# Performance work log

Measured on AMD Instinct MI355X. Metric: run time of the kernel, lower is better.

The kernel has to match this reference:

```python
import jax, jax.numpy as jnp
import numpy as np

N_NODES = 100000
N_EDGES = 1600000
IN_DIM = 128
HIDDEN = 128
OUT_DIM = 64


def setup_inputs() -> dict:
    key = jax.random.key(0)
    k_x, k_e, k_w1, k_b1, k_w2, k_b2 = jax.random.split(key, 6)
    x = jax.random.normal(k_x, (N_NODES, IN_DIM), dtype=jnp.float32)
    edge_index = jax.random.randint(k_e, (2, N_EDGES), 0, N_NODES, dtype=jnp.int64)
    # GCNConv weight/bias (glorot-ish scale) and final Linear head
    W1 = jax.random.normal(k_w1, (IN_DIM, HIDDEN), dtype=jnp.float32) / np.sqrt(IN_DIM)
    b1 = jnp.zeros((HIDDEN,), dtype=jnp.float32)
    W2 = jax.random.normal(k_w2, (HIDDEN, OUT_DIM), dtype=jnp.float32) / np.sqrt(HIDDEN)
    b2 = jnp.zeros((OUT_DIM,), dtype=jnp.float32)
    return {"x": x, "W1": W1, "b1": b1, "W2": W2, "b2": b2, "edge_index": edge_index}


def _gcn_conv(x, W, b, src, dst, norm, n_nodes):
    # PyG GCNConv: linear transform, then sym-normalized neighbor aggregation
    h = x @ W                                   # (N, H) dense transform
    msg = h[src] * norm[:, None]                # (E+N, H) gather + scale
    out = jax.ops.segment_sum(msg, dst, num_segments=n_nodes)  # scatter-add
    return out + b


def reference(x, W1, b1, W2, b2, edge_index):
    n = x.shape[0]
    # add self-loops (PyG GCNConv default)
    loop = jnp.arange(n, dtype=edge_index.dtype)
    src = jnp.concatenate([edge_index[0], loop])
    dst = jnp.concatenate([edge_index[1], loop])
    # symmetric normalization D^{-1/2} A D^{-1/2}
    deg = jnp.zeros((n,), dtype=x.dtype).at[dst].add(1.0)
    dinv = jnp.where(deg > 0, jax.lax.rsqrt(jnp.maximum(deg, 1.0)), 0.0)
    norm = dinv[src] * dinv[dst]

    h = _gcn_conv(x, W1, b1, src, dst, norm, n)
    h = jax.nn.relu(h)
    # dropout: identity in eval/inference mode
    return h @ W2 + b2
```

## Files before the change

### kernel.cpp

```cpp
#include <hip/hip_runtime.h>

#define N_NODES 100000
#define N_EDGES 1600000
#define IN_DIM  128
#define HIDDEN  128
#define OUT_DIM 64

#define NB_COARSE ((N_NODES + 255) / 256)
#define EPB 4096
#define NBLK_E ((N_EDGES + EPB - 1) / EPB)
#define CAP 5120
#define PCAP 6912

typedef __attribute__((ext_vector_type(8))) short bf8_t;
typedef __attribute__((ext_vector_type(4))) float f4_t;

__device__ __forceinline__ ushort f2b(float f) {
    unsigned int u = __float_as_uint(f);
    u += 0x7fffu + ((u >> 16) & 1u);
    return (ushort)(u >> 16);
}
__device__ __forceinline__ float b2f_lo(unsigned int u) { return __uint_as_float(u << 16); }
__device__ __forceinline__ float b2f_hi(unsigned int u) { return __uint_as_float(u & 0xffff0000u); }


__global__ void k_zero(int* __restrict__ cursor, unsigned int* __restrict__ hz) {
    int t = threadIdx.x;
    if (t < NB_COARSE) cursor[t] = t * CAP;
    if (t >= NB_COARSE && t < NB_COARSE + 64)
        hz[(size_t)N_NODES * 64 + (t - NB_COARSE)] = 0u;
}


__global__ __launch_bounds__(256) void k_part(const int* __restrict__ ei,
                                              int* __restrict__ cursor,
                                              unsigned int* __restrict__ part) {
    __shared__ int lh[NB_COARSE];
    __shared__ int lbase[NB_COARSE];
    int t = threadIdx.x;
    for (int i = t; i < NB_COARSE; i += 256) lh[i] = 0;
    __syncthreads();
    int e0 = blockIdx.x * EPB;
    int srcv[EPB / 256], dstv[EPB / 256];
    #pragma unroll
    for (int j = 0; j < EPB / 256; j++) {
        int e = e0 + j * 256 + t;
        if (e < N_EDGES) {
            srcv[j] = ei[e];
            dstv[j] = ei[N_EDGES + e];
            atomicAdd(&lh[dstv[j] >> 8], 1);
        } else dstv[j] = -1;
    }
    __syncthreads();
    for (int i = t; i < NB_COARSE; i += 256) {
        int c = lh[i];
        lbase[i] = (c > 0) ? atomicAdd(&cursor[i], c) : 0;
        lh[i] = 0;
    }
    __syncthreads();
    #pragma unroll
    for (int j = 0; j < EPB / 256; j++) {
        if (dstv[j] >= 0) {
            int b = dstv[j] >> 8;
            int pos = lbase[b] + atomicAdd(&lh[b], 1);
            part[pos] = ((unsigned int)(dstv[j] & 255) << 24) | (unsigned int)srcv[j];
        }
    }
}


__global__ __launch_bounds__(256) void k_csr(const unsigned int* __restrict__ part,
                                             const int* __restrict__ cursor,
                                             int* __restrict__ offs,
                                             int* __restrict__ pcnt,
                                             float* __restrict__ dinv,
                                             int* __restrict__ ssrc) {
    __shared__ int ldeg[256], lsc[256], lcur[256], sob[256];
    __shared__ unsigned int stage[CAP];
    int t = threadIdx.x;
    int b = blockIdx.x;
    int rbeg = b * CAP;
    int cnt = cursor[b] - rbeg;
    int node0 = b << 8;
    ldeg[t] = 0;
    __syncthreads();
    for (int i = t; i < cnt; i += 256) {
        unsigned int u = part[rbeg + i];
        stage[i] = u;
        atomicAdd(&ldeg[u >> 24], 1);
    }
    __syncthreads();
    int v = ldeg[t];
    int pv = (v + 7) & ~7;
    lsc[t] = pv;
    __syncthreads();
    for (int off = 1; off < 256; off <<= 1) {
        int add = (t >= off) ? lsc[t - off] : 0;
        __syncthreads();
        lsc[t] += add;
        __syncthreads();
    }
    int ob = b * PCAP + (lsc[t] - pv);
    sob[t] = ob;
    lcur[t] = 0;
    if (node0 + t < N_NODES) {
        offs[node0 + t] = ob;
        pcnt[node0 + t] = pv;
        dinv[node0 + t] = rsqrtf((float)(v + 1));
    }
    __syncthreads();
    for (int i = t; i < cnt; i += 256) {
        unsigned int u = stage[i];
        int d = u >> 24;
        int pos = atomicAdd(&lcur[d], 1);
        ssrc[sob[d] + pos] = (int)(u & 0xFFFFFFu);
    }
    for (int i = v; i < pv; i++) ssrc[ob + i] = N_NODES;
}


template <int BN, bool A_BF16, bool OUT_BF16>
__global__ __launch_bounds__(256, 2) void k_mfma(const void* __restrict__ Av,
                                                 const float* __restrict__ W,
                                                 const float* __restrict__ bias,
                                                 const float* __restrict__ dinv,
                                                 void* __restrict__ Cv, int M) {
    constexpr int BM = 128, KK = 128, PAD = 8;
    constexpr int MF = (BN == 128) ? 4 : 2;
    constexpr int NF = 4;
    __shared__ ushort As[BM][KK + PAD];
    __shared__ ushort Bs[BN][KK + PAD];

    int tid = threadIdx.x;
    int row0 = blockIdx.x * BM;

    if (A_BF16) {
        const ushort* A = (const ushort*)Av;
        #pragma unroll
        for (int i = 0; i < 8; i++) {
            int li = tid + i * 256;
            int r = li >> 4, c8 = li & 15;
            int grow = row0 + r; if (grow > M - 1) grow = M - 1;
            uint4 v = *(const uint4*)(A + (size_t)grow * KK + c8 * 8);
            *(uint4*)&As[r][c8 * 8] = v;
        }
    } else {
        const float* A = (const float*)Av;
        #pragma unroll
        for (int i = 0; i < 16; i++) {
            int li = tid + i * 256;
            int r = li >> 5, c4 = li & 31;
            int grow = row0 + r; if (grow > M - 1) grow = M - 1;
            float4 v = *(const float4*)(A + (size_t)grow * KK + c4 * 4);
            ushort4 o;
            o.x = f2b(v.x); o.y = f2b(v.y); o.z = f2b(v.z); o.w = f2b(v.w);
            *(ushort4*)&As[r][c4 * 4] = o;
        }
    }
    #pragma unroll
    for (int i = 0; i < (KK * BN / 4) / 256; i++) {
        int li = tid + i * 256;
        int k = li / (BN / 4), n4 = li % (BN / 4);
        float4 v = *(const float4*)(W + (size_t)k * BN + n4 * 4);
        Bs[n4 * 4 + 0][k] = f2b(v.x);
        Bs[n4 * 4 + 1][k] = f2b(v.y);
        Bs[n4 * 4 + 2][k] = f2b(v.z);
        Bs[n4 * 4 + 3][k] = f2b(v.w);
    }
    __syncthreads();

    int wave = tid >> 6, lane = tid & 63;
    int lr = lane & 15, lq = lane >> 4;
    int wm0 = (BN == 128) ? (wave & 1) * 64 : wave * 32;
    int wn0 = (BN == 128) ? (wave >> 1) * 64 : 0;

    f4_t acc[MF][NF];
    #pragma unroll
    for (int mi = 0; mi < MF; mi++)
        #pragma unroll
        for (int ni = 0; ni < NF; ni++) acc[mi][ni] = (f4_t){0.f, 0.f, 0.f, 0.f};

    #pragma unroll
    for (int kb = 0; kb < 4; kb++) {
        bf8_t af[MF], bfr[NF];
        #pragma unroll
        for (int mi = 0; mi < MF; mi++)
            af[mi] = *(const bf8_t*)&As[wm0 + mi * 16 + lr][kb * 32 + lq * 8];
        #pragma unroll
        for (int ni = 0; ni < NF; ni++)
            bfr[ni] = *(const bf8_t*)&Bs[wn0 + ni * 16 + lr][kb * 32 + lq * 8];
        #pragma unroll
        for (int mi = 0; mi < MF; mi++)
            #pragma unroll
            for (int ni = 0; ni < NF; ni++)
                acc[mi][ni] = __builtin_amdgcn_mfma_f32_16x16x32_bf16(
                    af[mi], bfr[ni], acc[mi][ni], 0, 0, 0);
    }

    #pragma unroll
    for (int mi = 0; mi < MF; mi++) {
        #pragma unroll
        for (int r = 0; r < 4; r++) {
            int row = row0 + wm0 + mi * 16 + lq * 4 + r;
            if (row < M) {
                if (OUT_BF16) {
                    float dv = dinv[row];
                    ushort* C = (ushort*)Cv;
                    #pragma unroll
                    for (int ni = 0; ni < NF; ni++)
                        C[(size_t)row * BN + wn0 + ni * 16 + lr] = f2b(acc[mi][ni][r] * dv);
                } else {
                    float* C = (float*)Cv;
                    #pragma unroll
                    for (int ni = 0; ni < NF; ni++) {
                        int col = wn0 + ni * 16 + lr;
                        C[(size_t)row * BN + col] = acc[mi][ni][r] + bias[col];
                    }
                }
            }
        }
    }
}


__global__ __launch_bounds__(256) void k_agg(const ushort* __restrict__ h,
                                             const int* __restrict__ offs,
                                             const int* __restrict__ pcnt,
                                             const int* __restrict__ ssrc,
                                             const float* __restrict__ dinv,
                                             const float* __restrict__ b1,
                                             ushort* __restrict__ h2) {
    int wave = threadIdx.x >> 6;
    int lane = threadIdx.x & 63;
    int n = blockIdx.x * 4 + wave;
    if (n >= N_NODES) return;

    const unsigned int* hp = (const unsigned int*)h;
    int e0 = offs[n];
    int iters = pcnt[n] >> 3;
    const uint4* ip = (const uint4*)(ssrc + e0);

    float ax0 = 0.f, ay0 = 0.f, ax1 = 0.f, ay1 = 0.f;
    float ax2 = 0.f, ay2 = 0.f, ax3 = 0.f, ay3 = 0.f;
    uint4 i0, i1;
    if (iters > 0) { i0 = ip[0]; i1 = ip[1]; }
    for (int it = 0; it < iters; it++) {
        uint4 nx0 = i0, nx1 = i1;
        if (it + 1 < iters) { nx0 = ip[(it + 1) * 2]; nx1 = ip[(it + 1) * 2 + 1]; }
        unsigned int u0 = hp[i0.x * 64 + lane];
        unsigned int u1 = hp[i0.y * 64 + lane];
        unsigned int u2 = hp[i0.z * 64 + lane];
        unsigned int u3 = hp[i0.w * 64 + lane];
        unsigned int u4 = hp[i1.x * 64 + lane];
        unsigned int u5 = hp[i1.y * 64 + lane];
        unsigned int u6 = hp[i1.z * 64 + lane];
        unsigned int u7 = hp[i1.w * 64 + lane];
        ax0 += b2f_lo(u0); ay0 += b2f_hi(u0);
        ax1 += b2f_lo(u1); ay1 += b2f_hi(u1);
        ax2 += b2f_lo(u2); ay2 += b2f_hi(u2);
        ax3 += b2f_lo(u3); ay3 += b2f_hi(u3);
        ax0 += b2f_lo(u4); ay0 += b2f_hi(u4);
        ax1 += b2f_lo(u5); ay1 += b2f_hi(u5);
        ax2 += b2f_lo(u6); ay2 += b2f_hi(u6);
        ax3 += b2f_lo(u7); ay3 += b2f_hi(u7);
        i0 = nx0; i1 = nx1;
    }
    unsigned int us = hp[(size_t)n * 64 + lane];
    float dn = dinv[n];
    float rx = (ax0 + ax1 + ax2 + ax3 + b2f_lo(us)) * dn;
    float ry = (ay0 + ay1 + ay2 + ay3 + b2f_hi(us)) * dn;
    float2 bb = ((const float2*)b1)[lane];
    rx += bb.x; ry += bb.y;
    rx = rx > 0.f ? rx : 0.f;
    ry = ry > 0.f ? ry : 0.f;
    unsigned int o = ((unsigned int)f2b(ry) << 16) | (unsigned int)f2b(rx);
    ((unsigned int*)h2)[(size_t)n * 64 + lane] = o;
}


extern "C" void kernel_launch(void* const* d_in, const int* in_sizes, int n_in,
                              void* d_out, int out_size, void* d_ws, size_t ws_size,
                              hipStream_t stream) {
    const float* x  = (const float*)d_in[0];
    const float* W1 = (const float*)d_in[1];
    const float* b1 = (const float*)d_in[2];
    const float* W2 = (const float*)d_in[3];
    const float* b2 = (const float*)d_in[4];
    const int*   ei = (const int*)d_in[5];
    float* out = (float*)d_out;

    char* w = (char*)d_ws;
    size_t off = 0;
    auto alloc = [&](size_t bytes) -> void* {
        void* p = w + off;
        off += (bytes + 255) & ~(size_t)255;
        return p;
    };
    ushort* h      = (ushort*)alloc((size_t)(N_NODES + 1) * HIDDEN * 2);
    ushort* h2     = (ushort*)alloc((size_t)N_NODES * HIDDEN * 2);
    float* dinv    = (float*)alloc((size_t)N_NODES * 4);
    int*   offs    = (int*)alloc((size_t)N_NODES * 4);
    int*   pcnt    = (int*)alloc((size_t)N_NODES * 4);
    int*   ssrc    = (int*)alloc((size_t)NB_COARSE * PCAP * 4);
    unsigned int* part = (unsigned int*)alloc((size_t)NB_COARSE * CAP * 4);
    int*   cursor  = (int*)alloc((size_t)NB_COARSE * 4);

    k_zero<<<1, 512, 0, stream>>>(cursor, (unsigned int*)h);
    k_part<<<NBLK_E, 256, 0, stream>>>(ei, cursor, part);
    k_csr<<<NB_COARSE, 256, 0, stream>>>(part, cursor, offs, pcnt, dinv, ssrc);

    k_mfma<HIDDEN, false, true><<<(N_NODES + 127) / 128, 256, 0, stream>>>(
        x, W1, nullptr, dinv, h, N_NODES);
    k_agg<<<(N_NODES + 3) / 4, 256, 0, stream>>>(h, offs, pcnt, ssrc, dinv, b1, h2);
    k_mfma<OUT_DIM, true, false><<<(N_NODES + 127) / 128, 256, 0, stream>>>(
        h2, W2, b2, nullptr, out, N_NODES);
}
```

Before: 235.8 us.

## Fuse neighbor aggregation with the output linear layer via shared memory

The aggregation kernel and the second GEMM are merged into one kernel. Each 512-thread block aggregates 128 nodes, 16 per wave, and writes the bf16 ReLU results into shared memory. It then runs MFMA against W2 in place and writes the final output. This removes the h2 intermediate round trip through global memory and one kernel launch. In exchange, the grid shrinks to about 782 blocks that each process nodes serially, which lowers the number of gathers in flight and can unbalance load across blocks.

```diff
diff --git a/kernel.cpp b/kernel.cpp
--- a/kernel.cpp
+++ b/kernel.cpp
@@ -119,48 +119,31 @@
 }
 
 
-template <int BN, bool A_BF16, bool OUT_BF16>
-__global__ __launch_bounds__(256, 2) void k_mfma(const void* __restrict__ Av,
-                                                 const float* __restrict__ W,
-                                                 const float* __restrict__ bias,
-                                                 const float* __restrict__ dinv,
-                                                 void* __restrict__ Cv, int M) {
-    constexpr int BM = 128, KK = 128, PAD = 8;
-    constexpr int MF = (BN == 128) ? 4 : 2;
-    constexpr int NF = 4;
+__global__ __launch_bounds__(256, 2) void k_mfma1(const float* __restrict__ A,
+                                                  const float* __restrict__ W,
+                                                  const float* __restrict__ dinv,
+                                                  ushort* __restrict__ C, int M) {
+    constexpr int BM = 128, KK = 128, PAD = 8, BN = 128, MF = 4, NF = 4;
     __shared__ ushort As[BM][KK + PAD];
     __shared__ ushort Bs[BN][KK + PAD];
 
     int tid = threadIdx.x;
     int row0 = blockIdx.x * BM;
 
-    if (A_BF16) {
-        const ushort* A = (const ushort*)Av;
-        #pragma unroll
-        for (int i = 0; i < 8; i++) {
-            int li = tid + i * 256;
-            int r = li >> 4, c8 = li & 15;
-            int grow = row0 + r; if (grow > M - 1) grow = M - 1;
-            uint4 v = *(const uint4*)(A + (size_t)grow * KK + c8 * 8);
-            *(uint4*)&As[r][c8 * 8] = v;
-        }
-    } else {
-        const float* A = (const float*)Av;
-        #pragma unroll
-        for (int i = 0; i < 16; i++) {
-            int li = tid + i * 256;
-            int r = li >> 5, c4 = li & 31;
-            int grow = row0 + r; if (grow > M - 1) grow = M - 1;
-            float4 v = *(const float4*)(A + (size_t)grow * KK + c4 * 4);
-            ushort4 o;
-            o.x = f2b(v.x); o.y = f2b(v.y); o.z = f2b(v.z); o.w = f2b(v.w);
-            *(ushort4*)&As[r][c4 * 4] = o;
-        }
-    }
-    #pragma unroll
-    for (int i = 0; i < (KK * BN / 4) / 256; i++) {
+    #pragma unroll
+    for (int i = 0; i < 16; i++) {
         int li = tid + i * 256;
-        int k = li / (BN / 4), n4 = li % (BN / 4);
+        int r = li >> 5, c4 = li & 31;
+        int grow = row0 + r; if (grow > M - 1) grow = M - 1;
+        float4 v = *(const float4*)(A + (size_t)grow * KK + c4 * 4);
+        ushort4 o;
+        o.x = f2b(v.x); o.y = f2b(v.y); o.z = f2b(v.z); o.w = f2b(v.w);
+        *(ushort4*)&As[r][c4 * 4] = o;
+    }
+    #pragma unroll
+    for (int i = 0; i < 16; i++) {
+        int li = tid + i * 256;
+        int k = li >> 5, n4 = li & 31;
         float4 v = *(const float4*)(W + (size_t)k * BN + n4 * 4);
         Bs[n4 * 4 + 0][k] = f2b(v.x);
         Bs[n4 * 4 + 1][k] = f2b(v.y);
@@ -171,8 +154,8 @@
 
     int wave = tid >> 6, lane = tid & 63;
     int lr = lane & 15, lq = lane >> 4;
-    int wm0 = (BN == 128) ? (wave & 1) * 64 : wave * 32;
-    int wn0 = (BN == 128) ? (wave >> 1) * 64 : 0;
+    int wm0 = (wave & 1) * 64;
+    int wn0 = (wave >> 1) * 64;
 
     f4_t acc[MF][NF];
     #pragma unroll
@@ -203,78 +186,114 @@
         for (int r = 0; r < 4; r++) {
             int row = row0 + wm0 + mi * 16 + lq * 4 + r;
             if (row < M) {
-                if (OUT_BF16) {
-                    float dv = dinv[row];
-                    ushort* C = (ushort*)Cv;
-                    #pragma unroll
-                    for (int ni = 0; ni < NF; ni++)
-                        C[(size_t)row * BN + wn0 + ni * 16 + lr] = f2b(acc[mi][ni][r] * dv);
-                } else {
-                    float* C = (float*)Cv;
-                    #pragma unroll
-                    for (int ni = 0; ni < NF; ni++) {
-                        int col = wn0 + ni * 16 + lr;
-                        C[(size_t)row * BN + col] = acc[mi][ni][r] + bias[col];
-                    }
-                }
+                float dv = dinv[row];
+                #pragma unroll
+                for (int ni = 0; ni < NF; ni++)
+                    C[(size_t)row * BN + wn0 + ni * 16 + lr] = f2b(acc[mi][ni][r] * dv);
             }
         }
     }
 }
 
 
-__global__ __launch_bounds__(256) void k_agg(const ushort* __restrict__ h,
-                                             const int* __restrict__ offs,
-                                             const int* __restrict__ pcnt,
-                                             const int* __restrict__ ssrc,
-                                             const float* __restrict__ dinv,
-                                             const float* __restrict__ b1,
-                                             ushort* __restrict__ h2) {
-    int wave = threadIdx.x >> 6;
-    int lane = threadIdx.x & 63;
-    int n = blockIdx.x * 4 + wave;
-    if (n >= N_NODES) return;
+__global__ __launch_bounds__(512, 6) void k_aggmm(const ushort* __restrict__ h,
+                                                  const int* __restrict__ offs,
+                                                  const int* __restrict__ pcnt,
+                                                  const int* __restrict__ ssrc,
+                                                  const float* __restrict__ dinv,
+                                                  const float* __restrict__ b1,
+                                                  const float* __restrict__ W2,
+                                                  const float* __restrict__ b2,
+                                                  float* __restrict__ out, int M) {
+    constexpr int BM = 128, KK = 128, PAD = 8, BN = 64;
+    __shared__ ushort As[BM][KK + PAD];
+    __shared__ ushort Bs[BN][KK + PAD];
+
+    int tid = threadIdx.x;
+    int wave = tid >> 6, lane = tid & 63;
+    int row0 = blockIdx.x * BM;
+
+    #pragma unroll
+    for (int i = 0; i < 4; i++) {
+        int li = tid + i * 512;
+        int k = li >> 4, n4 = li & 15;
+        float4 v = *(const float4*)(W2 + (size_t)k * BN + n4 * 4);
+        Bs[n4 * 4 + 0][k] = f2b(v.x);
+        Bs[n4 * 4 + 1][k] = f2b(v.y);
+        Bs[n4 * 4 + 2][k] = f2b(v.z);
+        Bs[n4 * 4 + 3][k] = f2b(v.w);
+    }
 
     const unsigned int* hp = (const unsigned int*)h;
-    int e0 = offs[n];
-    int iters = pcnt[n] >> 3;
-    const uint4* ip = (const uint4*)(ssrc + e0);
-
-    float ax0 = 0.f, ay0 = 0.f, ax1 = 0.f, ay1 = 0.f;
-    float ax2 = 0.f, ay2 = 0.f, ax3 = 0.f, ay3 = 0.f;
-    uint4 i0, i1;
-    if (iters > 0) { i0 = ip[0]; i1 = ip[1]; }
-    for (int it = 0; it < iters; it++) {
-        uint4 nx0 = i0, nx1 = i1;
-        if (it + 1 < iters) { nx0 = ip[(it + 1) * 2]; nx1 = ip[(it + 1) * 2 + 1]; }
-        unsigned int u0 = hp[i0.x * 64 + lane];
-        unsigned int u1 = hp[i0.y * 64 + lane];
-        unsigned int u2 = hp[i0.z * 64 + lane];
-        unsigned int u3 = hp[i0.w * 64 + lane];
-        unsigned int u4 = hp[i1.x * 64 + lane];
-        unsigned int u5 = hp[i1.y * 64 + lane];
-        unsigned int u6 = hp[i1.z * 64 + lane];
-        unsigned int u7 = hp[i1.w * 64 + lane];
-        ax0 += b2f_lo(u0); ay0 += b2f_hi(u0);
-        ax1 += b2f_lo(u1); ay1 += b2f_hi(u1);
-        ax2 += b2f_lo(u2); ay2 += b2f_hi(u2);
-        ax3 += b2f_lo(u3); ay3 += b2f_hi(u3);
-        ax0 += b2f_lo(u4); ay0 += b2f_hi(u4);
-        ax1 += b2f_lo(u5); ay1 += b2f_hi(u5);
-        ax2 += b2f_lo(u6); ay2 += b2f_hi(u6);
-        ax3 += b2f_lo(u7); ay3 += b2f_hi(u7);
-        i0 = nx0; i1 = nx1;
-    }
-    unsigned int us = hp[(size_t)n * 64 + lane];
-    float dn = dinv[n];
-    float rx = (ax0 + ax1 + ax2 + ax3 + b2f_lo(us)) * dn;
-    float ry = (ay0 + ay1 + ay2 + ay3 + b2f_hi(us)) * dn;
     float2 bb = ((const float2*)b1)[lane];
-    rx += bb.x; ry += bb.y;
-    rx = rx > 0.f ? rx : 0.f;
-    ry = ry > 0.f ? ry : 0.f;
-    unsigned int o = ((unsigned int)f2b(ry) << 16) | (unsigned int)f2b(rx);
-    ((unsigned int*)h2)[(size_t)n * 64 + lane] = o;
+    #pragma unroll 1
+    for (int nn = 0; nn < 16; nn++) {
+        int r = wave * 16 + nn;
+        int n = row0 + r;
+        if (n >= M) break;
+        int e0 = offs[n];
+        int iters = pcnt[n] >> 3;
+        const uint4* ip = (const uint4*)(ssrc + e0);
+
+        float2 a0 = {0.f, 0.f}, a1 = {0.f, 0.f}, a2 = {0.f, 0.f}, a3 = {0.f, 0.f};
+        uint4 i0, i1;
+        if (iters > 0) { i0 = ip[0]; i1 = ip[1]; }
+        for (int it = 0; it < iters; it++) {
+            uint4 nx0 = i0, nx1 = i1;
+            if (it + 1 < iters) { nx0 = ip[(it + 1) * 2]; nx1 = ip[(it + 1) * 2 + 1]; }
+            unsigned int u0 = hp[i0.x * 64 + lane];
+            unsigned int u1 = hp[i0.y * 64 + lane];
+            unsigned int u2 = hp[i0.z * 64 + lane];
+            unsigned int u3 = hp[i0.w * 64 + lane];
+            unsigned int u4 = hp[i1.x * 64 + lane];
+            unsigned int u5 = hp[i1.y * 64 + lane];
+            unsigned int u6 = hp[i1.z * 64 + lane];
+            unsigned int u7 = hp[i1.w * 64 + lane];
+            a0.x += b2f_lo(u0); a0.y += b2f_hi(u0);
+            a1.x += b2f_lo(u1); a1.y += b2f_hi(u1);
+            a2.x += b2f_lo(u2); a2.y += b2f_hi(u2);
+            a3.x += b2f_lo(u3); a3.y += b2f_hi(u3);
+            a0.x += b2f_lo(u4); a0.y += b2f_hi(u4);
+            a1.x += b2f_lo(u5); a1.y += b2f_hi(u5);
+            a2.x += b2f_lo(u6); a2.y += b2f_hi(u6);
+            a3.x += b2f_lo(u7); a3.y += b2f_hi(u7);
+            i0 = nx0; i1 = nx1;
+        }
+        unsigned int us = hp[(size_t)n * 64 + lane];
+        float dn = dinv[n];
+        float rx = (a0.x + a1.x + a2.x + a3.x + b2f_lo(us)) * dn + bb.x;
+        float ry = (a0.y + a1.y + a2.y + a3.y + b2f_hi(us)) * dn + bb.y;
+        rx = rx > 0.f ? rx : 0.f;
+        ry = ry > 0.f ? ry : 0.f;
+        unsigned int o = ((unsigned int)f2b(ry) << 16) | (unsigned int)f2b(rx);
+        *(unsigned int*)&As[r][lane * 2] = o;
+    }
+    __syncthreads();
+
+    int lr = lane & 15, lq = lane >> 4;
+    f4_t acc[4];
+    #pragma unroll
+    for (int ni = 0; ni < 4; ni++) acc[ni] = (f4_t){0.f, 0.f, 0.f, 0.f};
+    #pragma unroll
+    for (int kb = 0; kb < 4; kb++) {
+        bf8_t af = *(const bf8_t*)&As[wave * 16 + lr][kb * 32 + lq * 8];
+        #pragma unroll
+        for (int ni = 0; ni < 4; ni++) {
+            bf8_t bf = *(const bf8_t*)&Bs[ni * 16 + lr][kb * 32 + lq * 8];
+            acc[ni] = __builtin_amdgcn_mfma_f32_16x16x32_bf16(af, bf, acc[ni], 0, 0, 0);
+        }
+    }
+    #pragma unroll
+    for (int r = 0; r < 4; r++) {
+        int row = row0 + wave * 16 + lq * 4 + r;
+        if (row < M) {
+            #pragma unroll
+            for (int ni = 0; ni < 4; ni++) {
+                int col = ni * 16 + lr;
+                out[(size_t)row * BN + col] = acc[ni][r] + b2[col];
+            }
+        }
+    }
 }
 
 
@@ -297,7 +316,6 @@
         return p;
     };
     ushort* h      = (ushort*)alloc((size_t)(N_NODES + 1) * HIDDEN * 2);
-    ushort* h2     = (ushort*)alloc((size_t)N_NODES * HIDDEN * 2);
     float* dinv    = (float*)alloc((size_t)N_NODES * 4);
     int*   offs    = (int*)alloc((size_t)N_NODES * 4);
     int*   pcnt    = (int*)alloc((size_t)N_NODES * 4);
@@ -309,9 +327,7 @@
     k_part<<<NBLK_E, 256, 0, stream>>>(ei, cursor, part);
     k_csr<<<NB_COARSE, 256, 0, stream>>>(part, cursor, offs, pcnt, dinv, ssrc);
 
-    k_mfma<HIDDEN, false, true><<<(N_NODES + 127) / 128, 256, 0, stream>>>(
-        x, W1, nullptr, dinv, h, N_NODES);
-    k_agg<<<(N_NODES + 3) / 4, 256, 0, stream>>>(h, offs, pcnt, ssrc, dinv, b1, h2);
-    k_mfma<OUT_DIM, true, false><<<(N_NODES + 127) / 128, 256, 0, stream>>>(
-        h2, W2, b2, nullptr, out, N_NODES);
-}
+    k_mfma1<<<(N_NODES + 127) / 128, 256, 0, stream>>>(x, W1, dinv, h, N_NODES);
+    k_aggmm<<<(N_NODES + 127) / 128, 512, 0, stream>>>(h, offs, pcnt, ssrc, dinv,
+                                                       b1, W2, b2, out, N_NODES);
+}
```

New measurement: 255.6 us. +8.4%, slower.

## Fuse edge partitioning with first GEMM and move source-side normalization into aggregation

Applied to the files above, without the earlier changes.

The edge-partition kernel and the first X@W1 GEMM are merged into one launch that assigns blocks to either task, so the GEMM no longer waits for the CSR build and the two run concurrently. To allow that, the GEMM no longer scales rows by dinv. The aggregation kernel now gathers dinv[src] per neighbor and applies it with an FMA, and the self-loop term gets dinv applied twice. The zero-init kernel becomes a memset, and padding now relies on dinv[N_NODES]=0 instead of a zeroed h row. The cost is an extra random dinv gather per edge in the aggregation hot loop.

```diff
diff --git a/kernel.cpp b/kernel.cpp
--- a/kernel.cpp
+++ b/kernel.cpp
@@ -9,6 +9,7 @@
 #define NB_COARSE ((N_NODES + 255) / 256)
 #define EPB 4096
 #define NBLK_E ((N_EDGES + EPB - 1) / EPB)
+#define GB1 ((N_NODES + 127) / 128)
 #define CAP 5120
 #define PCAP 6912
 
@@ -24,46 +25,115 @@
 __device__ __forceinline__ float b2f_hi(unsigned int u) { return __uint_as_float(u & 0xffff0000u); }
 
 
-__global__ void k_zero(int* __restrict__ cursor, unsigned int* __restrict__ hz) {
-    int t = threadIdx.x;
-    if (t < NB_COARSE) cursor[t] = t * CAP;
-    if (t >= NB_COARSE && t < NB_COARSE + 64)
-        hz[(size_t)N_NODES * 64 + (t - NB_COARSE)] = 0u;
-}
-
-
-__global__ __launch_bounds__(256) void k_part(const int* __restrict__ ei,
-                                              int* __restrict__ cursor,
-                                              unsigned int* __restrict__ part) {
-    __shared__ int lh[NB_COARSE];
-    __shared__ int lbase[NB_COARSE];
-    int t = threadIdx.x;
-    for (int i = t; i < NB_COARSE; i += 256) lh[i] = 0;
-    __syncthreads();
-    int e0 = blockIdx.x * EPB;
-    int srcv[EPB / 256], dstv[EPB / 256];
-    #pragma unroll
-    for (int j = 0; j < EPB / 256; j++) {
-        int e = e0 + j * 256 + t;
-        if (e < N_EDGES) {
-            srcv[j] = ei[e];
-            dstv[j] = ei[N_EDGES + e];
-            atomicAdd(&lh[dstv[j] >> 8], 1);
-        } else dstv[j] = -1;
-    }
-    __syncthreads();
-    for (int i = t; i < NB_COARSE; i += 256) {
-        int c = lh[i];
-        lbase[i] = (c > 0) ? atomicAdd(&cursor[i], c) : 0;
-        lh[i] = 0;
-    }
-    __syncthreads();
-    #pragma unroll
-    for (int j = 0; j < EPB / 256; j++) {
-        if (dstv[j] >= 0) {
-            int b = dstv[j] >> 8;
-            int pos = lbase[b] + atomicAdd(&lh[b], 1);
-            part[pos] = ((unsigned int)(dstv[j] & 255) << 24) | (unsigned int)srcv[j];
+__global__ __launch_bounds__(256, 2) void k_fuse1(const int* __restrict__ ei,
+                                                  int* __restrict__ cursor,
+                                                  unsigned int* __restrict__ part,
+                                                  const float* __restrict__ x,
+                                                  const float* __restrict__ W1,
+                                                  ushort* __restrict__ h) {
+    __shared__ __align__(16) ushort smem[2 * 128 * 136];
+    int tid = threadIdx.x;
+
+    if (blockIdx.x < NBLK_E) {
+        int* lh    = (int*)smem;
+        int* lbase = lh + NB_COARSE;
+        for (int i = tid; i < NB_COARSE; i += 256) lh[i] = 0;
+        __syncthreads();
+        int e0 = blockIdx.x * EPB;
+        int srcv[EPB / 256], dstv[EPB / 256];
+        #pragma unroll
+        for (int j = 0; j < EPB / 256; j++) {
+            int e = e0 + j * 256 + tid;
+            if (e < N_EDGES) {
+                srcv[j] = ei[e];
+                dstv[j] = ei[N_EDGES + e];
+                atomicAdd(&lh[dstv[j] >> 8], 1);
+            } else dstv[j] = -1;
+        }
+        __syncthreads();
+        for (int i = tid; i < NB_COARSE; i += 256) {
+            int c = lh[i];
+            lbase[i] = (c > 0) ? (i * CAP + atomicAdd(&cursor[i], c)) : 0;
+            lh[i] = 0;
+        }
+        __syncthreads();
+        #pragma unroll
+        for (int j = 0; j < EPB / 256; j++) {
+            if (dstv[j] >= 0) {
+                int b = dstv[j] >> 8;
+                int pos = lbase[b] + atomicAdd(&lh[b], 1);
+                part[pos] = ((unsigned int)(dstv[j] & 255) << 24) | (unsigned int)srcv[j];
+            }
+        }
+        return;
+    }
+
+    typedef ushort (*tile_t)[136];
+    tile_t As = (tile_t)smem;
+    tile_t Bs = (tile_t)(smem + 128 * 136);
+    int row0 = (blockIdx.x - NBLK_E) * 128;
+    const int M = N_NODES;
+
+    #pragma unroll
+    for (int i = 0; i < 16; i++) {
+        int li = tid + i * 256;
+        int r = li >> 5, c4 = li & 31;
+        int grow = row0 + r; if (grow > M - 1) grow = M - 1;
+        float4 v = *(const float4*)(x + (size_t)grow * 128 + c4 * 4);
+        ushort4 o;
+        o.x = f2b(v.x); o.y = f2b(v.y); o.z = f2b(v.z); o.w = f2b(v.w);
+        *(ushort4*)&As[r][c4 * 4] = o;
+    }
+    #pragma unroll
+    for (int i = 0; i < 16; i++) {
+        int li = tid + i * 256;
+        int k = li >> 5, n4 = li & 31;
+        float4 v = *(const float4*)(W1 + (size_t)k * 128 + n4 * 4);
+        Bs[n4 * 4 + 0][k] = f2b(v.x);
+        Bs[n4 * 4 + 1][k] = f2b(v.y);
+        Bs[n4 * 4 + 2][k] = f2b(v.z);
+        Bs[n4 * 4 + 3][k] = f2b(v.w);
+    }
+    __syncthreads();
+
+    int wave = tid >> 6, lane = tid & 63;
+    int lr = lane & 15, lq = lane >> 4;
+    int wm0 = (wave & 1) * 64;
+    int wn0 = (wave >> 1) * 64;
+
+    f4_t acc[4][4];
+    #pragma unroll
+    for (int mi = 0; mi < 4; mi++)
+        #pragma unroll
+        for (int ni = 0; ni < 4; ni++) acc[mi][ni] = (f4_t){0.f, 0.f, 0.f, 0.f};
+
+    #pragma unroll
+    for (int kb = 0; kb < 4; kb++) {
+        bf8_t af[4], bfr[4];
+        #pragma unroll
+        for (int mi = 0; mi < 4; mi++)
+            af[mi] = *(const bf8_t*)&As[wm0 + mi * 16 + lr][kb * 32 + lq * 8];
+        #pragma unroll
+        for (int ni = 0; ni < 4; ni++)
+            bfr[ni] = *(const bf8_t*)&Bs[wn0 + ni * 16 + lr][kb * 32 + lq * 8];
+        #pragma unroll
+        for (int mi = 0; mi < 4; mi++)
+            #pragma unroll
+            for (int ni = 0; ni < 4; ni++)
+                acc[mi][ni] = __builtin_amdgcn_mfma_f32_16x16x32_bf16(
+                    af[mi], bfr[ni], acc[mi][ni], 0, 0, 0);
+    }
+
+    #pragma unroll
+    for (int mi = 0; mi < 4; mi++) {
+        #pragma unroll
+        for (int r = 0; r < 4; r++) {
+            int row = row0 + wm0 + mi * 16 + lq * 4 + r;
+            if (row < M) {
+                #pragma unroll
+                for (int ni = 0; ni < 4; ni++)
+                    h[(size_t)row * 128 + wn0 + ni * 16 + lr] = f2b(acc[mi][ni][r]);
+            }
         }
     }
 }
@@ -80,8 +150,9 @@
     int t = threadIdx.x;
     int b = blockIdx.x;
     int rbeg = b * CAP;
-    int cnt = cursor[b] - rbeg;
+    int cnt = cursor[b];
     int node0 = b << 8;
+    if (b == 0 && t == 0) dinv[N_NODES] = 0.f;
     ldeg[t] = 0;
     __syncthreads();
     for (int i = t; i < cnt; i += 256) {
@@ -116,110 +187,6 @@
         ssrc[sob[d] + pos] = (int)(u & 0xFFFFFFu);
     }
     for (int i = v; i < pv; i++) ssrc[ob + i] = N_NODES;
-}
-
-
-template <int BN, bool A_BF16, bool OUT_BF16>
-__global__ __launch_bounds__(256, 2) void k_mfma(const void* __restrict__ Av,
-                                                 const float* __restrict__ W,
-                                                 const float* __restrict__ bias,
-                                                 const float* __restrict__ dinv,
-                                                 void* __restrict__ Cv, int M) {
-    constexpr int BM = 128, KK = 128, PAD = 8;
-    constexpr int MF = (BN == 128) ? 4 : 2;
-    constexpr int NF = 4;
-    __shared__ ushort As[BM][KK + PAD];
-    __shared__ ushort Bs[BN][KK + PAD];
-
-    int tid = threadIdx.x;
-    int row0 = blockIdx.x * BM;
-
-    if (A_BF16) {
-        const ushort* A = (const ushort*)Av;
-        #pragma unroll
-        for (int i = 0; i < 8; i++) {
-            int li = tid + i * 256;
-            int r = li >> 4, c8 = li & 15;
-            int grow = row0 + r; if (grow > M - 1) grow = M - 1;
-            uint4 v = *(const uint4*)(A + (size_t)grow * KK + c8 * 8);
-            *(uint4*)&As[r][c8 * 8] = v;
-        }
-    } else {
-        const float* A = (const float*)Av;
-        #pragma unroll
-        for (int i = 0; i < 16; i++) {
-            int li = tid + i * 256;
-            int r = li >> 5, c4 = li & 31;
-            int grow = row0 + r; if (grow > M - 1) grow = M - 1;
-            float4 v = *(const float4*)(A + (size_t)grow * KK + c4 * 4);
-            ushort4 o;
-            o.x = f2b(v.x); o.y = f2b(v.y); o.z = f2b(v.z); o.w = f2b(v.w);
-            *(ushort4*)&As[r][c4 * 4] = o;
-        }
-    }
-    #pragma unroll
-    for (int i = 0; i < (KK * BN / 4) / 256; i++) {
-        int li = tid + i * 256;
-        int k = li / (BN / 4), n4 = li % (BN / 4);
-        float4 v = *(const float4*)(W + (size_t)k * BN + n4 * 4);
-        Bs[n4 * 4 + 0][k] = f2b(v.x);
-        Bs[n4 * 4 + 1][k] = f2b(v.y);
-        Bs[n4 * 4 + 2][k] = f2b(v.z);
-        Bs[n4 * 4 + 3][k] = f2b(v.w);
-    }
-    __syncthreads();
-
-    int wave = tid >> 6, lane = tid & 63;
-    int lr = lane & 15, lq = lane >> 4;
-    int wm0 = (BN == 128) ? (wave & 1) * 64 : wave * 32;
-    int wn0 = (BN == 128) ? (wave >> 1) * 64 : 0;
-
-    f4_t acc[MF][NF];
-    #pragma unroll
-    for (int mi = 0; mi < MF; mi++)
-        #pragma unroll
-        for (int ni = 0; ni < NF; ni++) acc[mi][ni] = (f4_t){0.f, 0.f, 0.f, 0.f};
-
-    #pragma unroll
-    for (int kb = 0; kb < 4; kb++) {
-        bf8_t af[MF], bfr[NF];
-        #pragma unroll
-        for (int mi = 0; mi < MF; mi++)
-            af[mi] = *(const bf8_t*)&As[wm0 + mi * 16 + lr][kb * 32 + lq * 8];
-        #pragma unroll
-        for (int ni = 0; ni < NF; ni++)
-            bfr[ni] = *(const bf8_t*)&Bs[wn0 + ni * 16 + lr][kb * 32 + lq * 8];
-        #pragma unroll
-        for (int mi = 0; mi < MF; mi++)
-            #pragma unroll
-            for (int ni = 0; ni < NF; ni++)
-                acc[mi][ni] = __builtin_amdgcn_mfma_f32_16x16x32_bf16(
-                    af[mi], bfr[ni], acc[mi][ni], 0, 0, 0);
-    }
-
-    #pragma unroll
-    for (int mi = 0; mi < MF; mi++) {
-        #pragma unroll
-        for (int r = 0; r < 4; r++) {
-            int row = row0 + wm0 + mi * 16 + lq * 4 + r;
-            if (row < M) {
-                if (OUT_BF16) {
-                    float dv = dinv[row];
-                    ushort* C = (ushort*)Cv;
-                    #pragma unroll
-                    for (int ni = 0; ni < NF; ni++)
-                        C[(size_t)row * BN + wn0 + ni * 16 + lr] = f2b(acc[mi][ni][r] * dv);
-                } else {
-                    float* C = (float*)Cv;
-                    #pragma unroll
-                    for (int ni = 0; ni < NF; ni++) {
-                        int col = wn0 + ni * 16 + lr;
-                        C[(size_t)row * BN + col] = acc[mi][ni][r] + bias[col];
-                    }
-                }
-            }
-        }
-    }
 }
 
 
@@ -247,6 +214,8 @@
     for (int it = 0; it < iters; it++) {
         uint4 nx0 = i0, nx1 = i1;
         if (it + 1 < iters) { nx0 = ip[(it + 1) * 2]; nx1 = ip[(it + 1) * 2 + 1]; }
+        float w0 = dinv[i0.x], w1 = dinv[i0.y], w2 = dinv[i0.z], w3 = dinv[i0.w];
+        float w4 = dinv[i1.x], w5 = dinv[i1.y], w6 = dinv[i1.z], w7 = dinv[i1.w];
         unsigned int u0 = hp[i0.x * 64 + lane];
         unsigned int u1 = hp[i0.y * 64 + lane];
         unsigned int u2 = hp[i0.z * 64 + lane];
@@ -255,26 +224,101 @@
         unsigned int u5 = hp[i1.y * 64 + lane];
         unsigned int u6 = hp[i1.z * 64 + lane];
         unsigned int u7 = hp[i1.w * 64 + lane];
-        ax0 += b2f_lo(u0); ay0 += b2f_hi(u0);
-        ax1 += b2f_lo(u1); ay1 += b2f_hi(u1);
-        ax2 += b2f_lo(u2); ay2 += b2f_hi(u2);
-        ax3 += b2f_lo(u3); ay3 += b2f_hi(u3);
-        ax0 += b2f_lo(u4); ay0 += b2f_hi(u4);
-        ax1 += b2f_lo(u5); ay1 += b2f_hi(u5);
-        ax2 += b2f_lo(u6); ay2 += b2f_hi(u6);
-        ax3 += b2f_lo(u7); ay3 += b2f_hi(u7);
+        ax0 = fmaf(b2f_lo(u0), w0, ax0); ay0 = fmaf(b2f_hi(u0), w0, ay0);
+        ax1 = fmaf(b2f_lo(u1), w1, ax1); ay1 = fmaf(b2f_hi(u1), w1, ay1);
+        ax2 = fmaf(b2f_lo(u2), w2, ax2); ay2 = fmaf(b2f_hi(u2), w2, ay2);
+        ax3 = fmaf(b2f_lo(u3), w3, ax3); ay3 = fmaf(b2f_hi(u3), w3, ay3);
+        ax0 = fmaf(b2f_lo(u4), w4, ax0); ay0 = fmaf(b2f_hi(u4), w4, ay0);
+        ax1 = fmaf(b2f_lo(u5), w5, ax1); ay1 = fmaf(b2f_hi(u5), w5, ay1);
+        ax2 = fmaf(b2f_lo(u6), w6, ax2); ay2 = fmaf(b2f_hi(u6), w6, ay2);
+        ax3 = fmaf(b2f_lo(u7), w7, ax3); ay3 = fmaf(b2f_hi(u7), w7, ay3);
         i0 = nx0; i1 = nx1;
     }
     unsigned int us = hp[(size_t)n * 64 + lane];
     float dn = dinv[n];
-    float rx = (ax0 + ax1 + ax2 + ax3 + b2f_lo(us)) * dn;
-    float ry = (ay0 + ay1 + ay2 + ay3 + b2f_hi(us)) * dn;
+    float rx = (ax0 + ax1 + ax2 + ax3 + b2f_lo(us) * dn) * dn;
+    float ry = (ay0 + ay1 + ay2 + ay3 + b2f_hi(us) * dn) * dn;
     float2 bb = ((const float2*)b1)[lane];
     rx += bb.x; ry += bb.y;
     rx = rx > 0.f ? rx : 0.f;
     ry = ry > 0.f ? ry : 0.f;
     unsigned int o = ((unsigned int)f2b(ry) << 16) | (unsigned int)f2b(rx);
     ((unsigned int*)h2)[(size_t)n * 64 + lane] = o;
+}
+
+
+__global__ __launch_bounds__(256, 2) void k_mfma2(const ushort* __restrict__ A,
+                                                  const float* __restrict__ W,
+                                                  const float* __restrict__ bias,
+                                                  float* __restrict__ C, int M) {
+    constexpr int BM = 128, KK = 128, PAD = 8, BN = 64, MF = 2, NF = 4;
+    __shared__ ushort As[BM][KK + PAD];
+    __shared__ ushort Bs[BN][KK + PAD];
+
+    int tid = threadIdx.x;
+    int row0 = blockIdx.x * BM;
+
+    #pragma unroll
+    for (int i = 0; i < 8; i++) {
+        int li = tid + i * 256;
+        int r = li >> 4, c8 = li & 15;
+        int grow = row0 + r; if (grow > M - 1) grow = M - 1;
+        uint4 v = *(const uint4*)(A + (size_t)grow * KK + c8 * 8);
+        *(uint4*)&As[r][c8 * 8] = v;
+    }
+    #pragma unroll
+    for (int i = 0; i < 8; i++) {
+        int li = tid + i * 256;
+        int k = li >> 4, n4 = li & 15;
+        float4 v = *(const float4*)(W + (size_t)k * BN + n4 * 4);
+        Bs[n4 * 4 + 0][k] = f2b(v.x);
+        Bs[n4 * 4 + 1][k] = f2b(v.y);
+        Bs[n4 * 4 + 2][k] = f2b(v.z);
+        Bs[n4 * 4 + 3][k] = f2b(v.w);
+    }
+    __syncthreads();
+
+    int wave = tid >> 6, lane = tid & 63;
+    int lr = lane & 15, lq = lane >> 4;
+    int wm0 = wave * 32;
+
+    f4_t acc[MF][NF];
+    #pragma unroll
+    for (int mi = 0; mi < MF; mi++)
+        #pragma unroll
+        for (int ni = 0; ni < NF; ni++) acc[mi][ni] = (f4_t){0.f, 0.f, 0.f, 0.f};
+
+    #pragma unroll
+    for (int kb = 0; kb < 4; kb++) {
+        bf8_t af[MF], bfr[NF];
+        #pragma unroll
+        for (int mi = 0; mi < MF; mi++)
+            af[mi] = *(const bf8_t*)&As[wm0 + mi * 16 + lr][kb * 32 + lq * 8];
+        #pragma unroll
+        for (int ni = 0; ni < NF; ni++)
+            bfr[ni] = *(const bf8_t*)&Bs[ni * 16 + lr][kb * 32 + lq * 8];
+        #pragma unroll
+        for (int mi = 0; mi < MF; mi++)
+            #pragma unroll
+            for (int ni = 0; ni < NF; ni++)
+                acc[mi][ni] = __builtin_amdgcn_mfma_f32_16x16x32_bf16(
+                    af[mi], bfr[ni], acc[mi][ni], 0, 0, 0);
+    }
+
+    #pragma unroll
+    for (int mi = 0; mi < MF; mi++) {
+        #pragma unroll
+        for (int r = 0; r < 4; r++) {
+            int row = row0 + wm0 + mi * 16 + lq * 4 + r;
+            if (row < M) {
+                #pragma unroll
+                for (int ni = 0; ni < NF; ni++) {
+                    int col = ni * 16 + lr;
+                    C[(size_t)row * BN + col] = acc[mi][ni][r] + bias[col];
+                }
+            }
+        }
+    }
 }
 
 
@@ -298,20 +342,16 @@
     };
     ushort* h      = (ushort*)alloc((size_t)(N_NODES + 1) * HIDDEN * 2);
     ushort* h2     = (ushort*)alloc((size_t)N_NODES * HIDDEN * 2);
-    float* dinv    = (float*)alloc((size_t)N_NODES * 4);
+    float* dinv    = (float*)alloc((size_t)(N_NODES + 1) * 4);
     int*   offs    = (int*)alloc((size_t)N_NODES * 4);
     int*   pcnt    = (int*)alloc((size_t)N_NODES * 4);
     int*   ssrc    = (int*)alloc((size_t)NB_COARSE * PCAP * 4);
     unsigned int* part = (unsigned int*)alloc((size_t)NB_COARSE * CAP * 4);
     int*   cursor  = (int*)alloc((size_t)NB_COARSE * 4);
 
-    k_zero<<<1, 512, 0, stream>>>(cursor, (unsigned int*)h);
-    k_part<<<NBLK_E, 256, 0, stream>>>(ei, cursor, part);
+    hipMemsetAsync(cursor, 0, (size_t)NB_COARSE * 4, stream);
+    k_fuse1<<<NBLK_E + GB1, 256, 0, stream>>>(ei, cursor, part, x, W1, h);
     k_csr<<<NB_COARSE, 256, 0, stream>>>(part, cursor, offs, pcnt, dinv, ssrc);
-
-    k_mfma<HIDDEN, false, true><<<(N_NODES + 127) / 128, 256, 0, stream>>>(
-        x, W1, nullptr, dinv, h, N_NODES);
     k_agg<<<(N_NODES + 3) / 4, 256, 0, stream>>>(h, offs, pcnt, ssrc, dinv, b1, h2);
-    k_mfma<OUT_DIM, true, false><<<(N_NODES + 127) / 128, 256, 0, stream>>>(
-        h2, W2, b2, nullptr, out, N_NODES);
-}
+    k_mfma2<<<GB1, 256, 0, stream>>>(h2, W2, b2, out, N_NODES);
+}
```

New measurement: 225.9 us. 1.04x faster.
